# Kernel optimization log

Hardware: AMD Instinct MI355X
Metric: run time of the kernel (lower is better)

## Reference

```python
import jax, jax.numpy as jnp
import numpy as np

N, E, G = 20480, 163840, 512          # nodes, edges, graphs
D, H, R, L = 128, 4, 8, 4             # embed dim, heads, relations, layers
HK = H * D                            # heads * out_channels (RGATConv internal width)
BOARD_WIDTH = 7
NEG_SLOPE = 0.2                       # RGATConv leaky_relu slope


def setup_inputs() -> dict:
    key = jax.random.key(0)
    ks = jax.random.split(key, 12)
    s_in = 1.0 / np.sqrt(D)
    s_att = 1.0 / np.sqrt(HK)
    return {
        "x_nodes": jax.random.randint(ks[0], (N,), 0, 3),
        "edge_index": jax.random.randint(ks[1], (2, E), 0, N),
        "edge_type": jax.random.randint(ks[2], (E,), 0, R),
        "batch": jnp.arange(N) // (N // G),  # G graphs of N//G nodes each
        "emb": jax.random.normal(ks[3], (3, D), jnp.float32),
        "W": jax.random.normal(ks[4], (L, R, D, HK), jnp.float32) * s_in,
        "Q": jax.random.normal(ks[5], (L, HK, H), jnp.float32) * s_att,
        "K": jax.random.normal(ks[6], (L, HK, H), jnp.float32) * s_att,
        "B": jnp.zeros((L, D), jnp.float32),
        "fc1_w": jax.random.normal(ks[7], (D, 64), jnp.float32) * s_in,
        "fc1_b": jnp.zeros((64,), jnp.float32),
        "pol_w": jax.random.normal(ks[8], (64, BOARD_WIDTH), jnp.float32) * 0.125,
        "pol_b": jnp.zeros((BOARD_WIDTH,), jnp.float32),
        "val_w": jax.random.normal(ks[9], (64, 1), jnp.float32) * 0.125,
        "val_b": jnp.zeros((1,), jnp.float32),
    }


def _rgat_layer(x, W, Q, Km, b, src, dst, etype):
    # RGATConv, additive-self-attention, across-relation softmax, concat=False.
    x_all = jnp.einsum('nd,rdk->nrk', x, W)          # [N,R,HK] per-relation transform
    q_all = jnp.einsum('nrk,kh->nrh', x_all, Q)      # [N,R,H]
    k_all = jnp.einsum('nrk,kh->nrh', x_all, Km)     # [N,R,H]
    alpha = jax.nn.leaky_relu(q_all[dst, etype] + k_all[src, etype], NEG_SLOPE)  # [E,H]
    # segment softmax over destination nodes (across all relations)
    amax = jax.lax.stop_gradient(jax.ops.segment_max(alpha, dst, num_segments=N))
    ex = jnp.exp(alpha - amax[dst])
    denom = jax.ops.segment_sum(ex, dst, num_segments=N)
    a = ex / (denom[dst] + 1e-16)                    # [E,H]
    msg = x_all[src, etype].reshape(E, H, D) * a[:, :, None]   # [E,H,D]
    agg = jax.ops.segment_sum(msg.reshape(E, HK), dst, num_segments=N)
    out = agg.reshape(N, H, D).mean(axis=1) + b      # head-mean (concat=False) + bias
    return jax.nn.relu(out)


def reference(x_nodes, edge_index, edge_type, batch, emb, W, Q, K, B,
              fc1_w, fc1_b, pol_w, pol_b, val_w, val_b):
    src, dst = edge_index[0], edge_index[1]
    x = emb[x_nodes]                                  # [N,D]
    for l in range(L):
        x = _rgat_layer(x, W[l], Q[l], K[l], B[l], src, dst, edge_type)
    cnt = jax.ops.segment_sum(jnp.ones((N,), x.dtype), batch, num_segments=G)
    pooled = jax.ops.segment_sum(x, batch, num_segments=G) / jnp.maximum(cnt, 1.0)[:, None]
    h = jax.nn.relu(pooled @ fc1_w + fc1_b)           # [G,64]
    policy = h @ pol_w + pol_b                        # [G,BOARD_WIDTH]
    value = jnp.tanh(h @ val_w + val_b)               # [G,1]
    return policy, value
```

## Files before the change

### kernel.cpp

```cpp
#include <hip/hip_runtime.h>
#include <cstdint>
#include <cstddef>

constexpr int N_  = 20480;
constexpr int E_  = 163840;
constexpr int G_  = 512;
constexpr int D_  = 128;
constexpr int H_  = 4;
constexpr int R_  = 8;
constexpr int L_  = 4;
constexpr int HK_ = 512;
constexpr int NPG_ = N_ / G_;

typedef short short8 __attribute__((ext_vector_type(8)));
typedef float f32x4 __attribute__((ext_vector_type(4)));
typedef unsigned short u16;
typedef unsigned int u32;

__device__ inline u16 bfr(float f) {
  u32 u = __builtin_bit_cast(u32, f);
  return (u16)((u + 0x7fffu + ((u >> 16) & 1u)) >> 16);
}
__device__ inline float bf2f(u32 lo16) { return __builtin_bit_cast(float, lo16 << 16); }
__device__ inline float lrelu(float v) { return v >= 0.f ? v : 0.2f * v; }

__global__ void k_zero2(int* __restrict__ cR, int* __restrict__ cN) {
  int i = blockIdx.x * blockDim.x + threadIdx.x;
  if (i < R_ * N_) cR[i] = 0;
  else if (i < R_ * N_ + N_) cN[i - R_ * N_] = 0;
}

__global__ void k_count_both(const int* __restrict__ dst, const int* __restrict__ et,
                             int* __restrict__ cR, int* __restrict__ cN) {
  int e = blockIdx.x * blockDim.x + threadIdx.x;
  if (e < E_) {
    int d = dst[e];
    atomicAdd(&cR[et[e] * N_ + d], 1);
    atomicAdd(&cN[d], 1);
  }
}

__global__ void k_bsum2(const int* __restrict__ cR, const int* __restrict__ cN,
                        int* __restrict__ bsumR, int* __restrict__ bsumN) {
  int b = blockIdx.x;
  const int* src = (b < 160) ? &cR[b * 1024] : &cN[(b - 160) * 1024];
  int t = threadIdx.x;
  const int4 v = *(const int4*)&src[t * 4];
  int s = v.x + v.y + v.z + v.w;
#pragma unroll
  for (int o = 32; o; o >>= 1) s += __shfl_down(s, o, 64);
  __shared__ int ws_[4];
  if ((t & 63) == 0) ws_[t >> 6] = s;
  __syncthreads();
  if (t == 0) {
    int tot = ws_[0] + ws_[1] + ws_[2] + ws_[3];
    if (b < 160) bsumR[b] = tot; else bsumN[b - 160] = tot;
  }
}

__global__ void k_bscan2(int* __restrict__ bsumR, int* __restrict__ bsumN,
                         int* __restrict__ totR, int* __restrict__ totN,
                         int* __restrict__ padBase) {
  __shared__ int shR[160];
  __shared__ int shN[20];
  int t = threadIdx.x;
  if (t < 160) shR[t] = bsumR[t];
  if (t < 20) shN[t] = bsumN[t];
  __syncthreads();
  if (t == 0) {
    int run = 0;
    for (int i = 0; i < 160; ++i) { int v = shR[i]; shR[i] = run; run += v; }
    totR[0] = run;
    int cum = 0;
    for (int r = 0; r < R_; ++r) {
      padBase[r] = cum;
      int lo = shR[r * 20];
      int hi = (r == R_ - 1) ? run : shR[(r + 1) * 20];
      cum += (hi - lo + 127) & ~127;
    }
    padBase[R_] = cum;
    int run2 = 0;
    for (int i = 0; i < 20; ++i) { int v = shN[i]; shN[i] = run2; run2 += v; }
    totN[0] = run2;
  }
  __syncthreads();
  if (t < 160) bsumR[t] = shR[t];
  if (t < 20) bsumN[t] = shN[t];
}

__global__ void k_scan32(const int* __restrict__ cR, const int* __restrict__ cN,
                         const int* __restrict__ bsumR, const int* __restrict__ bsumN,
                         int* __restrict__ ipR, int* __restrict__ curR,
                         int* __restrict__ ipN, int* __restrict__ curN) {
  __shared__ int ts[256];
  int b = blockIdx.x;
  const int* c;
  int off0;
  int* indptr;
  int* cursor;
  int lb;
  if (b < 160) { c = cR; off0 = bsumR[b]; indptr = ipR; cursor = curR; lb = b; }
  else { c = cN; off0 = bsumN[b - 160]; indptr = ipN; cursor = curN; lb = b - 160; }
  int t = threadIdx.x;
  int base = lb * 1024 + t * 4;
  const int4 v = *(const int4*)&c[base];
  int s0 = v.x, s01 = v.x + v.y, s012 = s01 + v.z, s = s012 + v.w;
  ts[t] = s;
  __syncthreads();
#pragma unroll
  for (int o = 1; o < 256; o <<= 1) {
    int add = (t >= o) ? ts[t - o] : 0;
    __syncthreads();
    ts[t] += add;
    __syncthreads();
  }
  int off = off0 + (t ? ts[t - 1] : 0);
  int4 o4 = make_int4(off, off + s0, off + s01, off + s012);
  *(int4*)&indptr[base] = o4;
  *(int4*)&cursor[base] = o4;
}

__global__ void k_scatter_both(const int* __restrict__ dst, const int* __restrict__ et,
                               const int* __restrict__ src, int* __restrict__ curR,
                               int* __restrict__ curN, int* __restrict__ slotOf,
                               int* __restrict__ srcR, int* __restrict__ esortD) {
  int e = blockIdx.x * blockDim.x + threadIdx.x;
  if (e < E_) {
    int d = dst[e];
    int p = atomicAdd(&curR[et[e] * N_ + d], 1);
    slotOf[e] = p;
    srcR[p] = src[e];
    int p2 = atomicAdd(&curN[d], 1);
    esortD[p2] = e;
  }
}

__global__ __launch_bounds__(256) void k_wqk_all(const float* __restrict__ W,
                                                 const float* __restrict__ Q,
                                                 const float* __restrict__ Km,
                                                 float* __restrict__ WQK) {
  int gw = (blockIdx.x * 256 + threadIdx.x) >> 6;
  int lane = threadIdx.x & 63;
  int d = gw & 127, r = (gw >> 7) & 7, l = gw >> 10;
  const float* wrow = W + (((size_t)l * R_ + r) * D_ + d) * HK_;
  const float* Ql = Q + (size_t)l * HK_ * H_;
  const float* Kl = Km + (size_t)l * HK_ * H_;
  float acc[8] = {0.f, 0.f, 0.f, 0.f, 0.f, 0.f, 0.f, 0.f};
#pragma unroll
  for (int it = 0; it < 8; ++it) {
    int k = it * 64 + lane;
    float w = wrow[k];
    const float4 qv = *(const float4*)&Ql[k * 4];
    const float4 kv = *(const float4*)&Kl[k * 4];
    acc[0] += w * qv.x; acc[1] += w * qv.y; acc[2] += w * qv.z; acc[3] += w * qv.w;
    acc[4] += w * kv.x; acc[5] += w * kv.y; acc[6] += w * kv.z; acc[7] += w * kv.w;
  }
#pragma unroll
  for (int o = 32; o; o >>= 1)
#pragma unroll
    for (int j = 0; j < 8; ++j) acc[j] += __shfl_down(acc[j], o, 64);
  if (lane == 0) {
#pragma unroll
    for (int h = 0; h < 4; ++h) {
      WQK[((size_t)l * D_ + d) * 64 + r * 4 + h] = acc[h];
      WQK[((size_t)l * D_ + d) * 64 + 32 + r * 4 + h] = acc[4 + h];
    }
  }
}

__global__ __launch_bounds__(256) void k_embed_qk(
    const int* __restrict__ xn, const float* __restrict__ emb,
    const float* __restrict__ WQK, float* __restrict__ x, u16* __restrict__ xb,
    float* __restrict__ q, float* __restrict__ kk) {
  __shared__ float xs[32][129];
  __shared__ float wq[128][64];
  __shared__ int xnl[32];
  const int t = threadIdx.x;
  const int n0 = blockIdx.x * 32;
  if (t < 32) xnl[t] = xn[n0 + t];
#pragma unroll
  for (int p = 0; p < 8; ++p) {
    int idx = t + p * 256;
    int row = idx >> 4, c4 = (idx & 15) * 4;
    *(float4*)&wq[row][c4] = *(const float4*)&WQK[row * 64 + c4];
  }
  __syncthreads();
#pragma unroll
  for (int p = 0; p < 16; ++p) {
    int idx = t + p * 256;
    int node = idx >> 7, d = idx & 127;
    float v = emb[xnl[node] * D_ + d];
    xs[node][d] = v;
    x[(size_t)(n0 + node) * D_ + d] = v;
    xb[(size_t)(n0 + node) * D_ + d] = bfr(v);
  }
  __syncthreads();
  const int node = t >> 3, cq = t & 7;
  float s[8];
#pragma unroll
  for (int j = 0; j < 8; ++j) s[j] = 0.f;
  for (int k = 0; k < 128; ++k) {
    float xv = xs[node][k];
#pragma unroll
    for (int j = 0; j < 8; ++j) s[j] = fmaf(xv, wq[k][cq * 8 + j], s[j]);
  }
#pragma unroll
  for (int j = 0; j < 8; ++j) {
    int c = cq * 8 + j;
    if (c < 32) q[(size_t)(n0 + node) * 32 + c] = s[j];
    else        kk[(size_t)(n0 + node) * 32 + (c - 32)] = s[j];
  }
}

__global__ __launch_bounds__(256) void k_attn(
    const int* __restrict__ ipN, const int* __restrict__ esD,
    const int* __restrict__ src, const int* __restrict__ et,
    const float* __restrict__ q, const float* __restrict__ kk,
    const int* __restrict__ slotOf, float* __restrict__ aw) {
  int n = blockIdx.x * 4 + (threadIdx.x >> 6);
  int lane = threadIdx.x & 63;
  int j0 = ipN[n], j1 = ipN[n + 1];
  int deg = j1 - j0;
  if (deg == 0) return;
  int h = lane & 3;
  if (deg <= 16) {
    int ei = lane >> 2;
    float a = -3.4e38f;
    int slot = 0;
    if (ei < deg) {
      int e = esD[j0 + ei];
      int r = et[e];
      slot = slotOf[e];
      a = lrelu(q[(size_t)n * 32 + r * 4 + h] + kk[(size_t)src[e] * 32 + r * 4 + h]);
    }
    float m = a;
#pragma unroll
    for (int o = 4; o < 64; o <<= 1) m = fmaxf(m, __shfl_xor(m, o, 64));
    float ex = (ei < deg) ? expf(a - m) : 0.f;
    float s = ex;
#pragma unroll
    for (int o = 4; o < 64; o <<= 1) s += __shfl_xor(s, o, 64);
    if (ei < deg) aw[(size_t)slot * 4 + h] = ex * (0.25f / (s + 1e-16f));
    return;
  }
  int nch = (deg + 15) >> 4;
  float m = -3.4e38f;
  for (int c = 0; c < nch; ++c) {
    int ei = c * 16 + (lane >> 2);
    if (ei < deg) {
      int e = esD[j0 + ei];
      int r = et[e];
      float a = lrelu(q[(size_t)n * 32 + r * 4 + h] + kk[(size_t)src[e] * 32 + r * 4 + h]);
      m = fmaxf(m, a);
    }
  }
#pragma unroll
  for (int o = 4; o < 64; o <<= 1) m = fmaxf(m, __shfl_xor(m, o, 64));
  float s = 0.f;
  for (int c = 0; c < nch; ++c) {
    int ei = c * 16 + (lane >> 2);
    if (ei < deg) {
      int e = esD[j0 + ei];
      int r = et[e];
      float a = lrelu(q[(size_t)n * 32 + r * 4 + h] + kk[(size_t)src[e] * 32 + r * 4 + h]);
      float ex = expf(a - m);
      s += ex;
      aw[(size_t)slotOf[e] * 4 + h] = ex;
    }
  }
#pragma unroll
  for (int o = 4; o < 64; o <<= 1) s += __shfl_xor(s, o, 64);
  float inv = 0.25f / (s + 1e-16f);
  for (int c = 0; c < nch; ++c) {
    int ei = c * 16 + (lane >> 2);
    if (ei < deg) {
      int e = esD[j0 + ei];
      aw[(size_t)slotOf[e] * 4 + h] *= inv;
    }
  }
}

__global__ void k_cvt_w_all(const float* __restrict__ W, u16* __restrict__ wt) {
  __shared__ u16 tile[64][65];
  const int z = blockIdx.z, k0 = blockIdx.y * 64, c0 = blockIdx.x * 64;
  const int t = threadIdx.x;
  const int tk = t >> 4, tc4 = (t & 15) * 4;
  const float* Wz = W + (size_t)z * D_ * HK_;
  u16* wz = wt + (size_t)z * HK_ * D_;
#pragma unroll
  for (int p = 0; p < 4; ++p) {
    int krow = tk + p * 16;
    const float4 v = *(const float4*)&Wz[(size_t)(k0 + krow) * HK_ + c0 + tc4];
    tile[tc4 + 0][krow] = bfr(v.x);
    tile[tc4 + 1][krow] = bfr(v.y);
    tile[tc4 + 2][krow] = bfr(v.z);
    tile[tc4 + 3][krow] = bfr(v.w);
  }
  __syncthreads();
#pragma unroll
  for (int p = 0; p < 4; ++p) {
    int crow = tk + p * 16;
    uint2 o;
    o.x = (u32)tile[crow][tc4 + 0] | ((u32)tile[crow][tc4 + 1] << 16);
    o.y = (u32)tile[crow][tc4 + 2] | ((u32)tile[crow][tc4 + 3] << 16);
    *(uint2*)&wz[(size_t)(c0 + crow) * D_ + k0 + tc4] = o;
  }
}

__global__ __launch_bounds__(512, 1) void k_edge8(
    const u16* __restrict__ xb, const u16* __restrict__ wt,
    const int* __restrict__ indptrR, const int* __restrict__ padBase,
    const int* __restrict__ srcR, const float* __restrict__ aw,
    u16* __restrict__ m) {
  __shared__ u16 atile[128 * 128];
  __shared__ u16 outb[128 * 128];
  __shared__ float awl[128][4];
  __shared__ int srcl[128];
  const int t = threadIdx.x;
  const int b128 = blockIdx.x * 128;
  if (b128 >= padBase[R_]) return;
  int r = 0;
  while (b128 >= padBase[r + 1]) ++r;
  const int ip0 = indptrR[r * N_];
  const int cnt = indptrR[(r + 1) * N_] - ip0;
  const int local0 = b128 - padBase[r];
  const u16* wrp = wt + (size_t)r * HK_ * D_;
  const int wid = t >> 6, lane = t & 63;
  const int l15 = lane & 15, l4 = lane >> 4;
  short8 breg[4][4];
#pragma unroll
  for (int ks = 0; ks < 4; ++ks)
#pragma unroll
    for (int h = 0; h < 4; ++h) {
      int c = (wid + 8 * h) * 16 + l15;
      breg[ks][h] = *(const short8*)(wrp + (size_t)c * 128 + ks * 32 + l4 * 8);
    }
  if (t < 128) {
    int lidx = local0 + t;
    if (lidx < cnt) {
      srcl[t] = srcR[ip0 + lidx];
      *(float4*)awl[t] = *(const float4*)(aw + (size_t)(ip0 + lidx) * 4);
    } else {
      srcl[t] = 0;
      *(float4*)awl[t] = make_float4(0.f, 0.f, 0.f, 0.f);
    }
  }
  __syncthreads();
#pragma unroll
  for (int p = 0; p < 4; ++p) {
    int idx = t + p * 512;
    int row = idx >> 4, seg = idx & 15;
    uint4 v = *(const uint4*)(xb + (size_t)srcl[row] * 128 + seg * 8);
    *(uint4*)((char*)atile + row * 256 + ((seg * 16) ^ ((row & 7) << 4))) = v;
  }
  __syncthreads();
  f32x4 acc[8][4];
#pragma unroll
  for (int i = 0; i < 8; ++i)
#pragma unroll
    for (int h = 0; h < 4; ++h) acc[i][h] = (f32x4){0.f, 0.f, 0.f, 0.f};
#pragma unroll
  for (int ks = 0; ks < 4; ++ks) {
    short8 av[8];
#pragma unroll
    for (int i = 0; i < 8; ++i) {
      int row = i * 16 + l15;
      av[i] = *(const short8*)((char*)atile + row * 256 +
                ((l4 * 16 + ks * 64) ^ ((row & 7) << 4)));
    }
#pragma unroll
    for (int i = 0; i < 8; ++i)
#pragma unroll
      for (int h = 0; h < 4; ++h)
        acc[i][h] = __builtin_amdgcn_mfma_f32_16x16x32_bf16(breg[ks][h], av[i],
                                                            acc[i][h], 0, 0, 0);
  }
#pragma unroll
  for (int i = 0; i < 8; ++i) {
    int row = i * 16 + l15;
    const float4 awf = *(const float4*)awl[row];
    float v0 = awf.x * acc[i][0][0] + awf.y * acc[i][1][0] + awf.z * acc[i][2][0] + awf.w * acc[i][3][0];
    float v1 = awf.x * acc[i][0][1] + awf.y * acc[i][1][1] + awf.z * acc[i][2][1] + awf.w * acc[i][3][1];
    float v2 = awf.x * acc[i][0][2] + awf.y * acc[i][1][2] + awf.z * acc[i][2][2] + awf.w * acc[i][3][2];
    float v3 = awf.x * acc[i][0][3] + awf.y * acc[i][1][3] + awf.z * acc[i][2][3] + awf.w * acc[i][3][3];
    uint2 o;
    o.x = (u32)bfr(v0) | ((u32)bfr(v1) << 16);
    o.y = (u32)bfr(v2) | ((u32)bfr(v3) << 16);
    *(uint2*)((char*)outb + row * 256 + ((wid * 32 + l4 * 8) ^ ((row & 7) << 4))) = o;
  }
  __syncthreads();
  {
    int row = t >> 2, c0 = (t & 3) * 64;
    char* gout = (char*)(m + (size_t)(b128 + row) * 128) + c0;
#pragma unroll
    for (int qq = 0; qq < 4; ++qq) {
      uint4 v = *(const uint4*)((char*)outb + row * 256 + ((c0 + qq * 16) ^ ((row & 7) << 4)));
      *(uint4*)(gout + qq * 16) = v;
    }
  }
}

__global__ __launch_bounds__(256) void k_aggqk(
    const int* __restrict__ indptrR, const int* __restrict__ padBase,
    const u16* __restrict__ m, const float* __restrict__ Bl,
    const float* __restrict__ WQK, int doqk,
    float* __restrict__ xout, u16* __restrict__ xbout,
    float* __restrict__ q, float* __restrict__ kk) {
  __shared__ float wqs[128 * 64];
  __shared__ float xrow[4][128];
  const int t = threadIdx.x;
  if (doqk) {
#pragma unroll
    for (int p = 0; p < 8; ++p)
      *(float4*)&wqs[(t + p * 256) * 4] = *(const float4*)&WQK[(t + p * 256) * 4];
  }
  const int w = t >> 6;
  int n = blockIdx.x * 4 + w;
  int lane = t & 63;
  float s0 = 0.f, s1 = 0.f;
#pragma unroll
  for (int r = 0; r < R_; ++r) {
    int ip0 = indptrR[r * N_];
    int j0 = indptrR[r * N_ + n], j1 = indptrR[r * N_ + n + 1];
    int base = padBase[r] + (j0 - ip0);
    int cntn = j1 - j0;
    int j = 0;
    for (; j + 1 < cntn; j += 2) {
      u32 v0 = *((const u32*)(m + (size_t)(base + j) * 128) + lane);
      u32 v1 = *((const u32*)(m + (size_t)(base + j + 1) * 128) + lane);
      s0 += bf2f(v0 & 0xffffu) + bf2f(v1 & 0xffffu);
      s1 += bf2f(v0 >> 16) + bf2f(v1 >> 16);
    }
    if (j < cntn) {
      u32 v0 = *((const u32*)(m + (size_t)(base + j) * 128) + lane);
      s0 += bf2f(v0 & 0xffffu);
      s1 += bf2f(v0 >> 16);
    }
  }
  float2 o;
  o.x = fmaxf(s0 + Bl[2 * lane], 0.f);
  o.y = fmaxf(s1 + Bl[2 * lane + 1], 0.f);
  *((float2*)(xout + (size_t)n * D_) + lane) = o;
  ((u32*)(xbout + (size_t)n * D_))[lane] = (u32)bfr(o.x) | ((u32)bfr(o.y) << 16);
  if (doqk) {
    xrow[w][2 * lane] = o.x;
    xrow[w][2 * lane + 1] = o.y;
    __syncthreads();
    const float* xr = xrow[w];
    float s = 0.f;
#pragma unroll
    for (int d4 = 0; d4 < 32; ++d4) {
      const float4 xv = *(const float4*)&xr[d4 * 4];
      s += xv.x * wqs[(d4 * 4 + 0) * 64 + lane] + xv.y * wqs[(d4 * 4 + 1) * 64 + lane] +
           xv.z * wqs[(d4 * 4 + 2) * 64 + lane] + xv.w * wqs[(d4 * 4 + 3) * 64 + lane];
    }
    if (lane < 32) q[(size_t)n * 32 + lane] = s;
    else           kk[(size_t)n * 32 + (lane - 32)] = s;
  }
}

__global__ void k_pool(const float* __restrict__ x, float* __restrict__ pooled) {
  int i = blockIdx.x * blockDim.x + threadIdx.x;
  if (i >= G_ * D_) return;
  int d = i & 127, g = i >> 7;
  float s = 0.f;
  for (int j = 0; j < NPG_; ++j) s += x[(size_t)(g * NPG_ + j) * D_ + d];
  pooled[i] = s * (1.0f / NPG_);
}

__global__ void k_head(const float* __restrict__ pooled, const float* __restrict__ fc1w,
                       const float* __restrict__ fc1b, const float* __restrict__ polw,
                       const float* __restrict__ polb, const float* __restrict__ valw,
                       const float* __restrict__ valb, float* __restrict__ out) {
  int g = blockIdx.x;
  int t = threadIdx.x;
  __shared__ float hb[64];
  const float* p = pooled + (size_t)g * D_;
  float s = fc1b[t];
  for (int d = 0; d < D_; ++d) s += p[d] * fc1w[d * 64 + t];
  hb[t] = fmaxf(s, 0.f);
  __syncthreads();
  if (t < 7) {
    float s2 = polb[t];
    for (int j = 0; j < 64; ++j) s2 += hb[j] * polw[j * 7 + t];
    out[g * 7 + t] = s2;
  } else if (t == 7) {
    float s2 = valb[0];
    for (int j = 0; j < 64; ++j) s2 += hb[j] * valw[j];
    out[G_ * 7 + g] = tanhf(s2);
  }
}

extern "C" void kernel_launch(void* const* d_in, const int* in_sizes, int n_in,
                              void* d_out, int out_size, void* d_ws, size_t ws_size,
                              hipStream_t stream) {
  (void)in_sizes; (void)n_in; (void)out_size;
  const int*   x_nodes = (const int*)d_in[0];
  const int*   eidx    = (const int*)d_in[1];
  const int*   etype   = (const int*)d_in[2];
  const float* emb     = (const float*)d_in[4];
  const float* W       = (const float*)d_in[5];
  const float* Q       = (const float*)d_in[6];
  const float* Km      = (const float*)d_in[7];
  const float* B       = (const float*)d_in[8];
  const float* fc1w    = (const float*)d_in[9];
  const float* fc1b    = (const float*)d_in[10];
  const float* polw    = (const float*)d_in[11];
  const float* polb    = (const float*)d_in[12];
  const float* valw    = (const float*)d_in[13];
  const float* valb    = (const float*)d_in[14];
  float* out = (float*)d_out;
  const int* srcA = eidx;
  const int* dstA = eidx + E_;

  char* p = (char*)d_ws;
  size_t used = 0;
  auto carve = [&](size_t bytes) {
    char* q = p;
    size_t adv = (bytes + 255) & ~(size_t)255;
    p += adv;
    used += adv;
    return q;
  };
  float* x_cur  = (float*)carve((size_t)N_ * D_ * 4);
  float* x_nxt  = (float*)carve((size_t)N_ * D_ * 4);
  u16*   xbf    = (u16*)carve((size_t)N_ * D_ * 2);
  u16*   mbuf   = (u16*)carve((size_t)(E_ + R_ * 128) * D_ * 2);
  float* qbuf   = (float*)carve((size_t)N_ * 32 * 4);
  float* kbuf   = (float*)carve((size_t)N_ * 32 * 4);
  float* awbuf  = (float*)carve((size_t)E_ * H_ * 4);
  float* WQKb   = (float*)carve((size_t)L_ * D_ * 64 * 4);
  u16*   Wtb    = (u16*)carve((size_t)L_ * R_ * HK_ * D_ * 2);
  float* pooled = (float*)carve((size_t)G_ * D_ * 4);
  int* countsR  = (int*)carve((size_t)R_ * N_ * 4);
  int* cursorR  = (int*)carve((size_t)R_ * N_ * 4);
  int* indptrR  = (int*)carve((size_t)(R_ * N_ + 1) * 4);
  int* slotOf   = (int*)carve((size_t)E_ * 4);
  int* srcR     = (int*)carve((size_t)E_ * 4);
  int* countsN  = (int*)carve((size_t)N_ * 4);
  int* cursorN  = (int*)carve((size_t)N_ * 4);
  int* indptrN  = (int*)carve((size_t)(N_ + 1) * 4);
  int* esortD   = (int*)carve((size_t)E_ * 4);
  int* padBase  = (int*)carve((size_t)(R_ + 1) * 4);
  int* bsumR    = (int*)carve((size_t)160 * 4);
  int* bsumN    = (int*)carve((size_t)32 * 4);
  if (used > ws_size) return;

  constexpr int RN = R_ * N_;
  constexpr int EDGE_BLOCKS = E_ / 128 + R_;

  k_zero2<<<(RN + N_ + 255) / 256, 256, 0, stream>>>(countsR, countsN);
  k_count_both<<<E_ / 256, 256, 0, stream>>>(dstA, etype, countsR, countsN);
  k_bsum2<<<180, 256, 0, stream>>>(countsR, countsN, bsumR, bsumN);
  k_bscan2<<<1, 256, 0, stream>>>(bsumR, bsumN, indptrR + RN, indptrN + N_, padBase);
  k_scan32<<<180, 256, 0, stream>>>(countsR, countsN, bsumR, bsumN,
                                    indptrR, cursorR, indptrN, cursorN);
  k_scatter_both<<<E_ / 256, 256, 0, stream>>>(dstA, etype, srcA, cursorR, cursorN,
                                               slotOf, srcR, esortD);
  k_wqk_all<<<(L_ * R_ * D_ * 64) / 256, 256, 0, stream>>>(W, Q, Km, WQKb);
  k_cvt_w_all<<<dim3(HK_ / 64, D_ / 64, L_ * R_), 256, 0, stream>>>(W, Wtb);
  k_embed_qk<<<N_ / 32, 256, 0, stream>>>(x_nodes, emb, WQKb, x_cur, xbf, qbuf, kbuf);

  for (int l = 0; l < L_; ++l) {
    const float* Bl = B + (size_t)l * D_;
    k_attn<<<N_ / 4, 256, 0, stream>>>(indptrN, esortD, srcA, etype, qbuf, kbuf,
                                       slotOf, awbuf);
    k_edge8<<<EDGE_BLOCKS, 512, 0, stream>>>(xbf, Wtb + (size_t)l * R_ * HK_ * D_,
                                             indptrR, padBase, srcR, awbuf, mbuf);
    int doqk = (l < L_ - 1) ? 1 : 0;
    k_aggqk<<<N_ / 4, 256, 0, stream>>>(indptrR, padBase, mbuf, Bl,
                                        WQKb + (size_t)(l + 1) * D_ * 64 * (doqk ? 1 : 0),
                                        doqk, x_nxt, xbf, qbuf, kbuf);
    float* tmp = x_cur; x_cur = x_nxt; x_nxt = tmp;
  }

  k_pool<<<(G_ * D_) / 256, 256, 0, stream>>>(x_cur, pooled);
  k_head<<<G_, 64, 0, stream>>>(pooled, fc1w, fc1b, polw, polb, valw, valb, out);
}
```

Before: 502.3 us.

## Aggregate attention-weighted inputs per node and relation before the weight matmul

Replaces the per-edge transform kernel plus the separate aggregation kernel with one node-centric kernel. Each block of 32 nodes first sums the attention-weighted source features per relation and head, then multiplies the aggregate by the relation weight with MFMA. This moves the matmul from per edge to per node and relation, and the per-edge bf16 message buffer is no longer written or read. In exchange the relation weights are re-read from global memory by every block, and the gather loop is scalar and unbalanced across nodes with different degrees.

```diff
diff --git a/kernel.cpp b/kernel.cpp
--- a/kernel.cpp
+++ b/kernel.cpp
@@ -59,8 +59,7 @@
 }
 
 __global__ void k_bscan2(int* __restrict__ bsumR, int* __restrict__ bsumN,
-                         int* __restrict__ totR, int* __restrict__ totN,
-                         int* __restrict__ padBase) {
+                         int* __restrict__ totR, int* __restrict__ totN) {
   __shared__ int shR[160];
   __shared__ int shN[20];
   int t = threadIdx.x;
@@ -71,14 +70,6 @@
     int run = 0;
     for (int i = 0; i < 160; ++i) { int v = shR[i]; shR[i] = run; run += v; }
     totR[0] = run;
-    int cum = 0;
-    for (int r = 0; r < R_; ++r) {
-      padBase[r] = cum;
-      int lo = shR[r * 20];
-      int hi = (r == R_ - 1) ? run : shR[(r + 1) * 20];
-      cum += (hi - lo + 127) & ~127;
-    }
-    padBase[R_] = cum;
     int run2 = 0;
     for (int i = 0; i < 20; ++i) { int v = shN[i]; shN[i] = run2; run2 += v; }
     totN[0] = run2;
@@ -307,155 +298,146 @@
   }
 }
 
-__global__ __launch_bounds__(512, 1) void k_edge8(
+__global__ __launch_bounds__(256, 2) void k_node(
     const u16* __restrict__ xb, const u16* __restrict__ wt,
-    const int* __restrict__ indptrR, const int* __restrict__ padBase,
-    const int* __restrict__ srcR, const float* __restrict__ aw,
-    u16* __restrict__ m) {
-  __shared__ u16 atile[128 * 128];
-  __shared__ u16 outb[128 * 128];
-  __shared__ float awl[128][4];
-  __shared__ int srcl[128];
-  const int t = threadIdx.x;
-  const int b128 = blockIdx.x * 128;
-  if (b128 >= padBase[R_]) return;
-  int r = 0;
-  while (b128 >= padBase[r + 1]) ++r;
-  const int ip0 = indptrR[r * N_];
-  const int cnt = indptrR[(r + 1) * N_] - ip0;
-  const int local0 = b128 - padBase[r];
-  const u16* wrp = wt + (size_t)r * HK_ * D_;
-  const int wid = t >> 6, lane = t & 63;
-  const int l15 = lane & 15, l4 = lane >> 4;
-  short8 breg[4][4];
-#pragma unroll
-  for (int ks = 0; ks < 4; ++ks)
-#pragma unroll
-    for (int h = 0; h < 4; ++h) {
-      int c = (wid + 8 * h) * 16 + l15;
-      breg[ks][h] = *(const short8*)(wrp + (size_t)c * 128 + ks * 32 + l4 * 8);
-    }
-  if (t < 128) {
-    int lidx = local0 + t;
-    if (lidx < cnt) {
-      srcl[t] = srcR[ip0 + lidx];
-      *(float4*)awl[t] = *(const float4*)(aw + (size_t)(ip0 + lidx) * 4);
-    } else {
-      srcl[t] = 0;
-      *(float4*)awl[t] = make_float4(0.f, 0.f, 0.f, 0.f);
-    }
-  }
-  __syncthreads();
-#pragma unroll
-  for (int p = 0; p < 4; ++p) {
-    int idx = t + p * 512;
-    int row = idx >> 4, seg = idx & 15;
-    uint4 v = *(const uint4*)(xb + (size_t)srcl[row] * 128 + seg * 8);
-    *(uint4*)((char*)atile + row * 256 + ((seg * 16) ^ ((row & 7) << 4))) = v;
-  }
-  __syncthreads();
-  f32x4 acc[8][4];
-#pragma unroll
-  for (int i = 0; i < 8; ++i)
-#pragma unroll
-    for (int h = 0; h < 4; ++h) acc[i][h] = (f32x4){0.f, 0.f, 0.f, 0.f};
-#pragma unroll
-  for (int ks = 0; ks < 4; ++ks) {
-    short8 av[8];
-#pragma unroll
-    for (int i = 0; i < 8; ++i) {
-      int row = i * 16 + l15;
-      av[i] = *(const short8*)((char*)atile + row * 256 +
-                ((l4 * 16 + ks * 64) ^ ((row & 7) << 4)));
-    }
-#pragma unroll
-    for (int i = 0; i < 8; ++i)
-#pragma unroll
-      for (int h = 0; h < 4; ++h)
-        acc[i][h] = __builtin_amdgcn_mfma_f32_16x16x32_bf16(breg[ks][h], av[i],
-                                                            acc[i][h], 0, 0, 0);
-  }
-#pragma unroll
-  for (int i = 0; i < 8; ++i) {
-    int row = i * 16 + l15;
-    const float4 awf = *(const float4*)awl[row];
-    float v0 = awf.x * acc[i][0][0] + awf.y * acc[i][1][0] + awf.z * acc[i][2][0] + awf.w * acc[i][3][0];
-    float v1 = awf.x * acc[i][0][1] + awf.y * acc[i][1][1] + awf.z * acc[i][2][1] + awf.w * acc[i][3][1];
-    float v2 = awf.x * acc[i][0][2] + awf.y * acc[i][1][2] + awf.z * acc[i][2][2] + awf.w * acc[i][3][2];
-    float v3 = awf.x * acc[i][0][3] + awf.y * acc[i][1][3] + awf.z * acc[i][2][3] + awf.w * acc[i][3][3];
-    uint2 o;
-    o.x = (u32)bfr(v0) | ((u32)bfr(v1) << 16);
-    o.y = (u32)bfr(v2) | ((u32)bfr(v3) << 16);
-    *(uint2*)((char*)outb + row * 256 + ((wid * 32 + l4 * 8) ^ ((row & 7) << 4))) = o;
-  }
-  __syncthreads();
-  {
-    int row = t >> 2, c0 = (t & 3) * 64;
-    char* gout = (char*)(m + (size_t)(b128 + row) * 128) + c0;
-#pragma unroll
-    for (int qq = 0; qq < 4; ++qq) {
-      uint4 v = *(const uint4*)((char*)outb + row * 256 + ((c0 + qq * 16) ^ ((row & 7) << 4)));
-      *(uint4*)(gout + qq * 16) = v;
-    }
-  }
-}
-
-__global__ __launch_bounds__(256) void k_aggqk(
-    const int* __restrict__ indptrR, const int* __restrict__ padBase,
-    const u16* __restrict__ m, const float* __restrict__ Bl,
+    const int* __restrict__ ipR, const int* __restrict__ srcR,
+    const float* __restrict__ aw, const float* __restrict__ Bl,
     const float* __restrict__ WQK, int doqk,
     float* __restrict__ xout, u16* __restrict__ xbout,
     float* __restrict__ q, float* __restrict__ kk) {
-  __shared__ float wqs[128 * 64];
-  __shared__ float xrow[4][128];
+  __shared__ u16 Y[4][32 * 128];
+  __shared__ float xrow[32][132];
+  float* wqs = (float*)&Y[0][0];
   const int t = threadIdx.x;
+  const int n0 = blockIdx.x * 32;
+  const int nl = t >> 3, sl = t & 7;
+  const int w = t >> 6, lane = t & 63;
+  const int l15 = lane & 15, l4 = lane >> 4;
+  f32x4 acc[2][2];
+#pragma unroll
+  for (int i = 0; i < 2; ++i)
+#pragma unroll
+    for (int fi = 0; fi < 2; ++fi) acc[i][fi] = (f32x4){0.f, 0.f, 0.f, 0.f};
+
+  for (int r = 0; r < R_; ++r) {
+    int j0 = ipR[r * N_ + n0 + nl];
+    int j1 = ipR[r * N_ + n0 + nl + 1];
+    float y[4][16];
+#pragma unroll
+    for (int h = 0; h < 4; ++h)
+#pragma unroll
+      for (int d = 0; d < 16; ++d) y[h][d] = 0.f;
+    for (int j = j0; j < j1; ++j) {
+      int s = srcR[j];
+      const float4 a4 = *(const float4*)(aw + (size_t)j * 4);
+      const uint4 xv0 = *(const uint4*)(xb + (size_t)s * 128 + sl * 16);
+      const uint4 xv1 = *(const uint4*)(xb + (size_t)s * 128 + sl * 16 + 8);
+      float xf[16];
+      xf[0] = bf2f(xv0.x & 0xffffu); xf[1] = bf2f(xv0.x >> 16);
+      xf[2] = bf2f(xv0.y & 0xffffu); xf[3] = bf2f(xv0.y >> 16);
+      xf[4] = bf2f(xv0.z & 0xffffu); xf[5] = bf2f(xv0.z >> 16);
+      xf[6] = bf2f(xv0.w & 0xffffu); xf[7] = bf2f(xv0.w >> 16);
+      xf[8] = bf2f(xv1.x & 0xffffu); xf[9] = bf2f(xv1.x >> 16);
+      xf[10] = bf2f(xv1.y & 0xffffu); xf[11] = bf2f(xv1.y >> 16);
+      xf[12] = bf2f(xv1.z & 0xffffu); xf[13] = bf2f(xv1.z >> 16);
+      xf[14] = bf2f(xv1.w & 0xffffu); xf[15] = bf2f(xv1.w >> 16);
+#pragma unroll
+      for (int d = 0; d < 16; ++d) {
+        y[0][d] = fmaf(a4.x, xf[d], y[0][d]);
+        y[1][d] = fmaf(a4.y, xf[d], y[1][d]);
+        y[2][d] = fmaf(a4.z, xf[d], y[2][d]);
+        y[3][d] = fmaf(a4.w, xf[d], y[3][d]);
+      }
+    }
+    __syncthreads();
+#pragma unroll
+    for (int h = 0; h < 4; ++h) {
+      uint4 o0, o1;
+      o0.x = (u32)bfr(y[h][0]) | ((u32)bfr(y[h][1]) << 16);
+      o0.y = (u32)bfr(y[h][2]) | ((u32)bfr(y[h][3]) << 16);
+      o0.z = (u32)bfr(y[h][4]) | ((u32)bfr(y[h][5]) << 16);
+      o0.w = (u32)bfr(y[h][6]) | ((u32)bfr(y[h][7]) << 16);
+      o1.x = (u32)bfr(y[h][8]) | ((u32)bfr(y[h][9]) << 16);
+      o1.y = (u32)bfr(y[h][10]) | ((u32)bfr(y[h][11]) << 16);
+      o1.z = (u32)bfr(y[h][12]) | ((u32)bfr(y[h][13]) << 16);
+      o1.w = (u32)bfr(y[h][14]) | ((u32)bfr(y[h][15]) << 16);
+      char* base = (char*)Y[h] + nl * 256;
+      *(uint4*)(base + ((sl * 32 + 0) ^ ((nl & 7) << 4))) = o0;
+      *(uint4*)(base + ((sl * 32 + 16) ^ ((nl & 7) << 4))) = o1;
+    }
+    __syncthreads();
+    const u16* wrp = wt + (size_t)r * HK_ * D_;
+#pragma unroll
+    for (int h = 0; h < 4; ++h) {
+      short8 bv[2][4];
+#pragma unroll
+      for (int fi = 0; fi < 2; ++fi)
+#pragma unroll
+        for (int ks = 0; ks < 4; ++ks) {
+          int c = h * 128 + (w + 4 * fi) * 16 + l15;
+          bv[fi][ks] = *(const short8*)(wrp + (size_t)c * 128 + ks * 32 + l4 * 8);
+        }
+#pragma unroll
+      for (int ks = 0; ks < 4; ++ks) {
+        short8 av[2];
+#pragma unroll
+        for (int i = 0; i < 2; ++i) {
+          int row = i * 16 + l15;
+          av[i] = *(const short8*)((char*)Y[h] + row * 256 +
+                    ((l4 * 16 + ks * 64) ^ ((row & 7) << 4)));
+        }
+#pragma unroll
+        for (int i = 0; i < 2; ++i)
+#pragma unroll
+          for (int fi = 0; fi < 2; ++fi)
+            acc[i][fi] = __builtin_amdgcn_mfma_f32_16x16x32_bf16(bv[fi][ks], av[i],
+                                                                 acc[i][fi], 0, 0, 0);
+      }
+    }
+  }
+  __syncthreads();
+#pragma unroll
+  for (int i = 0; i < 2; ++i)
+#pragma unroll
+    for (int fi = 0; fi < 2; ++fi) {
+      int row = i * 16 + l15;
+      int cb = (w + 4 * fi) * 16 + l4 * 4;
+      float4 o;
+      o.x = fmaxf(acc[i][fi][0] + Bl[cb + 0], 0.f);
+      o.y = fmaxf(acc[i][fi][1] + Bl[cb + 1], 0.f);
+      o.z = fmaxf(acc[i][fi][2] + Bl[cb + 2], 0.f);
+      o.w = fmaxf(acc[i][fi][3] + Bl[cb + 3], 0.f);
+      *(float4*)&xrow[row][cb] = o;
+    }
   if (doqk) {
 #pragma unroll
-    for (int p = 0; p < 8; ++p)
-      *(float4*)&wqs[(t + p * 256) * 4] = *(const float4*)&WQK[(t + p * 256) * 4];
-  }
-  const int w = t >> 6;
-  int n = blockIdx.x * 4 + w;
-  int lane = t & 63;
-  float s0 = 0.f, s1 = 0.f;
-#pragma unroll
-  for (int r = 0; r < R_; ++r) {
-    int ip0 = indptrR[r * N_];
-    int j0 = indptrR[r * N_ + n], j1 = indptrR[r * N_ + n + 1];
-    int base = padBase[r] + (j0 - ip0);
-    int cntn = j1 - j0;
-    int j = 0;
-    for (; j + 1 < cntn; j += 2) {
-      u32 v0 = *((const u32*)(m + (size_t)(base + j) * 128) + lane);
-      u32 v1 = *((const u32*)(m + (size_t)(base + j + 1) * 128) + lane);
-      s0 += bf2f(v0 & 0xffffu) + bf2f(v1 & 0xffffu);
-      s1 += bf2f(v0 >> 16) + bf2f(v1 >> 16);
-    }
-    if (j < cntn) {
-      u32 v0 = *((const u32*)(m + (size_t)(base + j) * 128) + lane);
-      s0 += bf2f(v0 & 0xffffu);
-      s1 += bf2f(v0 >> 16);
-    }
-  }
-  float2 o;
-  o.x = fmaxf(s0 + Bl[2 * lane], 0.f);
-  o.y = fmaxf(s1 + Bl[2 * lane + 1], 0.f);
-  *((float2*)(xout + (size_t)n * D_) + lane) = o;
-  ((u32*)(xbout + (size_t)n * D_))[lane] = (u32)bfr(o.x) | ((u32)bfr(o.y) << 16);
+    for (int p = 0; p < 32; ++p) wqs[t + p * 256] = WQK[t + p * 256];
+  }
+  __syncthreads();
+#pragma unroll
+  for (int pp = 0; pp < 8; ++pp) {
+    int idx = t + pp * 256;
+    int row = idx >> 6, c2 = (idx & 63) * 2;
+    float v0 = xrow[row][c2], v1 = xrow[row][c2 + 1];
+    *(float2*)(xout + (size_t)(n0 + row) * D_ + c2) = make_float2(v0, v1);
+    *((u32*)(xbout + (size_t)(n0 + row) * D_ + c2)) = (u32)bfr(v0) | ((u32)bfr(v1) << 16);
+  }
   if (doqk) {
-    xrow[w][2 * lane] = o.x;
-    xrow[w][2 * lane + 1] = o.y;
-    __syncthreads();
-    const float* xr = xrow[w];
-    float s = 0.f;
-#pragma unroll
-    for (int d4 = 0; d4 < 32; ++d4) {
-      const float4 xv = *(const float4*)&xr[d4 * 4];
-      s += xv.x * wqs[(d4 * 4 + 0) * 64 + lane] + xv.y * wqs[(d4 * 4 + 1) * 64 + lane] +
-           xv.z * wqs[(d4 * 4 + 2) * 64 + lane] + xv.w * wqs[(d4 * 4 + 3) * 64 + lane];
-    }
-    if (lane < 32) q[(size_t)n * 32 + lane] = s;
-    else           kk[(size_t)n * 32 + (lane - 32)] = s;
+    const int node = t >> 3, cq = t & 7;
+    float s[8];
+#pragma unroll
+    for (int j = 0; j < 8; ++j) s[j] = 0.f;
+    for (int k2 = 0; k2 < 128; ++k2) {
+      float xv = xrow[node][k2];
+#pragma unroll
+      for (int j = 0; j < 8; ++j) s[j] = fmaf(xv, wqs[k2 * 64 + cq * 8 + j], s[j]);
+    }
+#pragma unroll
+    for (int j = 0; j < 8; ++j) {
+      int c = cq * 8 + j;
+      if (c < 32) q[(size_t)(n0 + node) * 32 + c] = s[j];
+      else        kk[(size_t)(n0 + node) * 32 + (c - 32)] = s[j];
+    }
   }
 }
 
@@ -523,9 +505,8 @@
     return q;
   };
   float* x_cur  = (float*)carve((size_t)N_ * D_ * 4);
-  float* x_nxt  = (float*)carve((size_t)N_ * D_ * 4);
-  u16*   xbf    = (u16*)carve((size_t)N_ * D_ * 2);
-  u16*   mbuf   = (u16*)carve((size_t)(E_ + R_ * 128) * D_ * 2);
+  u16*   xbf_a  = (u16*)carve((size_t)N_ * D_ * 2);
+  u16*   xbf_b  = (u16*)carve((size_t)N_ * D_ * 2);
   float* qbuf   = (float*)carve((size_t)N_ * 32 * 4);
   float* kbuf   = (float*)carve((size_t)N_ * 32 * 4);
   float* awbuf  = (float*)carve((size_t)E_ * H_ * 4);
@@ -541,37 +522,36 @@
   int* cursorN  = (int*)carve((size_t)N_ * 4);
   int* indptrN  = (int*)carve((size_t)(N_ + 1) * 4);
   int* esortD   = (int*)carve((size_t)E_ * 4);
-  int* padBase  = (int*)carve((size_t)(R_ + 1) * 4);
   int* bsumR    = (int*)carve((size_t)160 * 4);
   int* bsumN    = (int*)carve((size_t)32 * 4);
   if (used > ws_size) return;
 
   constexpr int RN = R_ * N_;
-  constexpr int EDGE_BLOCKS = E_ / 128 + R_;
 
   k_zero2<<<(RN + N_ + 255) / 256, 256, 0, stream>>>(countsR, countsN);
   k_count_both<<<E_ / 256, 256, 0, stream>>>(dstA, etype, countsR, countsN);
   k_bsum2<<<180, 256, 0, stream>>>(countsR, countsN, bsumR, bsumN);
-  k_bscan2<<<1, 256, 0, stream>>>(bsumR, bsumN, indptrR + RN, indptrN + N_, padBase);
+  k_bscan2<<<1, 256, 0, stream>>>(bsumR, bsumN, indptrR + RN, indptrN + N_);
   k_scan32<<<180, 256, 0, stream>>>(countsR, countsN, bsumR, bsumN,
                                     indptrR, cursorR, indptrN, cursorN);
   k_scatter_both<<<E_ / 256, 256, 0, stream>>>(dstA, etype, srcA, cursorR, cursorN,
                                                slotOf, srcR, esortD);
   k_wqk_all<<<(L_ * R_ * D_ * 64) / 256, 256, 0, stream>>>(W, Q, Km, WQKb);
   k_cvt_w_all<<<dim3(HK_ / 64, D_ / 64, L_ * R_), 256, 0, stream>>>(W, Wtb);
-  k_embed_qk<<<N_ / 32, 256, 0, stream>>>(x_nodes, emb, WQKb, x_cur, xbf, qbuf, kbuf);
-
+  k_embed_qk<<<N_ / 32, 256, 0, stream>>>(x_nodes, emb, WQKb, x_cur, xbf_a, qbuf, kbuf);
+
+  u16* xb_cur = xbf_a;
+  u16* xb_nxt = xbf_b;
   for (int l = 0; l < L_; ++l) {
     const float* Bl = B + (size_t)l * D_;
+    int doqk = (l < L_ - 1) ? 1 : 0;
+    const float* WQKn = doqk ? (WQKb + (size_t)(l + 1) * D_ * 64) : WQKb;
     k_attn<<<N_ / 4, 256, 0, stream>>>(indptrN, esortD, srcA, etype, qbuf, kbuf,
                                        slotOf, awbuf);
-    k_edge8<<<EDGE_BLOCKS, 512, 0, stream>>>(xbf, Wtb + (size_t)l * R_ * HK_ * D_,
-                                             indptrR, padBase, srcR, awbuf, mbuf);
-    int doqk = (l < L_ - 1) ? 1 : 0;
-    k_aggqk<<<N_ / 4, 256, 0, stream>>>(indptrR, padBase, mbuf, Bl,
-                                        WQKb + (size_t)(l + 1) * D_ * 64 * (doqk ? 1 : 0),
-                                        doqk, x_nxt, xbf, qbuf, kbuf);
-    float* tmp = x_cur; x_cur = x_nxt; x_nxt = tmp;
+    k_node<<<N_ / 32, 256, 0, stream>>>(xb_cur, Wtb + (size_t)l * R_ * HK_ * D_,
+                                        indptrR, srcR, awbuf, Bl, WQKn, doqk,
+                                        x_cur, xb_nxt, qbuf, kbuf);
+    u16* tmp = xb_cur; xb_cur = xb_nxt; xb_nxt = tmp;
   }
 
   k_pool<<<(G_ * D_) / 256, 256, 0, stream>>>(x_cur, pooled);
```

After: 591.2 us. 17.7% more time.

## Scatter edge messages into destination-sorted order for contiguous aggregation

Applied to the files above, without the earlier changes.

The edge GEMM kernel now writes each message row to its destination-sorted slot, using a new per-edge map from relation-sorted position to destination-sorted position, instead of writing rows in relation-padded order. The aggregation kernel then reads one contiguous range per node via the node CSR rather than walking eight per-relation segments, which cuts index loads and loop overhead. The cost is that stores from the edge kernel become scattered 256-byte rows instead of coalesced contiguous tiles.

```diff
diff --git a/kernel.cpp b/kernel.cpp
--- a/kernel.cpp
+++ b/kernel.cpp
@@ -123,7 +123,8 @@
 __global__ void k_scatter_both(const int* __restrict__ dst, const int* __restrict__ et,
                                const int* __restrict__ src, int* __restrict__ curR,
                                int* __restrict__ curN, int* __restrict__ slotOf,
-                               int* __restrict__ srcR, int* __restrict__ esortD) {
+                               int* __restrict__ srcR, int* __restrict__ dstOf,
+                               int* __restrict__ esortD) {
   int e = blockIdx.x * blockDim.x + threadIdx.x;
   if (e < E_) {
     int d = dst[e];
@@ -132,6 +133,7 @@
     srcR[p] = src[e];
     int p2 = atomicAdd(&curN[d], 1);
     esortD[p2] = e;
+    dstOf[p] = p2;
   }
 }
 
@@ -310,12 +312,13 @@
 __global__ __launch_bounds__(512, 1) void k_edge8(
     const u16* __restrict__ xb, const u16* __restrict__ wt,
     const int* __restrict__ indptrR, const int* __restrict__ padBase,
-    const int* __restrict__ srcR, const float* __restrict__ aw,
-    u16* __restrict__ m) {
+    const int* __restrict__ srcR, const int* __restrict__ dstOf,
+    const float* __restrict__ aw, u16* __restrict__ m) {
   __shared__ u16 atile[128 * 128];
   __shared__ u16 outb[128 * 128];
   __shared__ float awl[128][4];
   __shared__ int srcl[128];
+  __shared__ int dsl[128];
   const int t = threadIdx.x;
   const int b128 = blockIdx.x * 128;
   if (b128 >= padBase[R_]) return;
@@ -339,9 +342,11 @@
     int lidx = local0 + t;
     if (lidx < cnt) {
       srcl[t] = srcR[ip0 + lidx];
+      dsl[t] = dstOf[ip0 + lidx];
       *(float4*)awl[t] = *(const float4*)(aw + (size_t)(ip0 + lidx) * 4);
     } else {
       srcl[t] = 0;
+      dsl[t] = -1;
       *(float4*)awl[t] = make_float4(0.f, 0.f, 0.f, 0.f);
     }
   }
@@ -391,19 +396,21 @@
   __syncthreads();
   {
     int row = t >> 2, c0 = (t & 3) * 64;
-    char* gout = (char*)(m + (size_t)(b128 + row) * 128) + c0;
-#pragma unroll
-    for (int qq = 0; qq < 4; ++qq) {
-      uint4 v = *(const uint4*)((char*)outb + row * 256 + ((c0 + qq * 16) ^ ((row & 7) << 4)));
-      *(uint4*)(gout + qq * 16) = v;
+    int slot = dsl[row];
+    if (slot >= 0) {
+      char* gout = (char*)(m + (size_t)slot * 128) + c0;
+#pragma unroll
+      for (int qq = 0; qq < 4; ++qq) {
+        uint4 v = *(const uint4*)((char*)outb + row * 256 + ((c0 + qq * 16) ^ ((row & 7) << 4)));
+        *(uint4*)(gout + qq * 16) = v;
+      }
     }
   }
 }
 
 __global__ __launch_bounds__(256) void k_aggqk(
-    const int* __restrict__ indptrR, const int* __restrict__ padBase,
-    const u16* __restrict__ m, const float* __restrict__ Bl,
-    const float* __restrict__ WQK, int doqk,
+    const int* __restrict__ ipN, const u16* __restrict__ m,
+    const float* __restrict__ Bl, const float* __restrict__ WQK, int doqk,
     float* __restrict__ xout, u16* __restrict__ xbout,
     float* __restrict__ q, float* __restrict__ kk) {
   __shared__ float wqs[128 * 64];
@@ -417,25 +424,19 @@
   const int w = t >> 6;
   int n = blockIdx.x * 4 + w;
   int lane = t & 63;
+  int j0 = ipN[n], j1 = ipN[n + 1];
   float s0 = 0.f, s1 = 0.f;
-#pragma unroll
-  for (int r = 0; r < R_; ++r) {
-    int ip0 = indptrR[r * N_];
-    int j0 = indptrR[r * N_ + n], j1 = indptrR[r * N_ + n + 1];
-    int base = padBase[r] + (j0 - ip0);
-    int cntn = j1 - j0;
-    int j = 0;
-    for (; j + 1 < cntn; j += 2) {
-      u32 v0 = *((const u32*)(m + (size_t)(base + j) * 128) + lane);
-      u32 v1 = *((const u32*)(m + (size_t)(base + j + 1) * 128) + lane);
-      s0 += bf2f(v0 & 0xffffu) + bf2f(v1 & 0xffffu);
-      s1 += bf2f(v0 >> 16) + bf2f(v1 >> 16);
-    }
-    if (j < cntn) {
-      u32 v0 = *((const u32*)(m + (size_t)(base + j) * 128) + lane);
-      s0 += bf2f(v0 & 0xffffu);
-      s1 += bf2f(v0 >> 16);
-    }
+  int j = j0;
+  for (; j + 1 < j1; j += 2) {
+    u32 v0 = *((const u32*)(m + (size_t)j * 128) + lane);
+    u32 v1 = *((const u32*)(m + (size_t)(j + 1) * 128) + lane);
+    s0 += bf2f(v0 & 0xffffu) + bf2f(v1 & 0xffffu);
+    s1 += bf2f(v0 >> 16) + bf2f(v1 >> 16);
+  }
+  if (j < j1) {
+    u32 v0 = *((const u32*)(m + (size_t)j * 128) + lane);
+    s0 += bf2f(v0 & 0xffffu);
+    s1 += bf2f(v0 >> 16);
   }
   float2 o;
   o.x = fmaxf(s0 + Bl[2 * lane], 0.f);
@@ -525,7 +526,7 @@
   float* x_cur  = (float*)carve((size_t)N_ * D_ * 4);
   float* x_nxt  = (float*)carve((size_t)N_ * D_ * 4);
   u16*   xbf    = (u16*)carve((size_t)N_ * D_ * 2);
-  u16*   mbuf   = (u16*)carve((size_t)(E_ + R_ * 128) * D_ * 2);
+  u16*   mbuf   = (u16*)carve((size_t)E_ * D_ * 2);
   float* qbuf   = (float*)carve((size_t)N_ * 32 * 4);
   float* kbuf   = (float*)carve((size_t)N_ * 32 * 4);
   float* awbuf  = (float*)carve((size_t)E_ * H_ * 4);
@@ -537,6 +538,7 @@
   int* indptrR  = (int*)carve((size_t)(R_ * N_ + 1) * 4);
   int* slotOf   = (int*)carve((size_t)E_ * 4);
   int* srcR     = (int*)carve((size_t)E_ * 4);
+  int* dstOf    = (int*)carve((size_t)E_ * 4);
   int* countsN  = (int*)carve((size_t)N_ * 4);
   int* cursorN  = (int*)carve((size_t)N_ * 4);
   int* indptrN  = (int*)carve((size_t)(N_ + 1) * 4);
@@ -556,7 +558,7 @@
   k_scan32<<<180, 256, 0, stream>>>(countsR, countsN, bsumR, bsumN,
                                     indptrR, cursorR, indptrN, cursorN);
   k_scatter_both<<<E_ / 256, 256, 0, stream>>>(dstA, etype, srcA, cursorR, cursorN,
-                                               slotOf, srcR, esortD);
+                                               slotOf, srcR, dstOf, esortD);
   k_wqk_all<<<(L_ * R_ * D_ * 64) / 256, 256, 0, stream>>>(W, Q, Km, WQKb);
   k_cvt_w_all<<<dim3(HK_ / 64, D_ / 64, L_ * R_), 256, 0, stream>>>(W, Wtb);
   k_embed_qk<<<N_ / 32, 256, 0, stream>>>(x_nodes, emb, WQKb, x_cur, xbf, qbuf, kbuf);
@@ -566,9 +568,9 @@
     k_attn<<<N_ / 4, 256, 0, stream>>>(indptrN, esortD, srcA, etype, qbuf, kbuf,
                                        slotOf, awbuf);
     k_edge8<<<EDGE_BLOCKS, 512, 0, stream>>>(xbf, Wtb + (size_t)l * R_ * HK_ * D_,
-                                             indptrR, padBase, srcR, awbuf, mbuf);
+                                             indptrR, padBase, srcR, dstOf, awbuf, mbuf);
     int doqk = (l < L_ - 1) ? 1 : 0;
-    k_aggqk<<<N_ / 4, 256, 0, stream>>>(indptrR, padBase, mbuf, Bl,
+    k_aggqk<<<N_ / 4, 256, 0, stream>>>(indptrN, mbuf, Bl,
                                         WQKb + (size_t)(l + 1) * D_ * 64 * (doqk ? 1 : 0),
                                         doqk, x_nxt, xbf, qbuf, kbuf);
     float* tmp = x_cur; x_cur = x_nxt; x_nxt = tmp;
```

New measurement: 454.2 us. -9.6%, faster.
